# Optimization experiments

Measured on AMD Instinct MI355X. Metric: run time of the kernel, lower is better.

Reference implementation:

```python
import jax, jax.numpy as jnp
import numpy as np

EPS = 1e-12  # F.normalize default eps


def setup_inputs() -> dict:
    key = jax.random.key(0)
    k1, k2 = jax.random.split(key)
    E, N, B, T, Fdim, K = 2, 512, 64, 12, 2, 64
    supports = jax.random.uniform(k1, (E, N, N), dtype=jnp.float32)
    inputs = jax.random.normal(k2, (B, T, N, Fdim), dtype=jnp.float32)
    bias = jnp.ones((E, K), dtype=jnp.float32)  # init.ones_
    # torch.svd at __init__: A = u @ diag(s) @ v^T, truncated to node_dim
    u_np, s_np, vh_np = np.linalg.svd(np.asarray(supports), full_matrices=False)
    u = jnp.asarray(u_np[..., :K])                      # [E, N, K]
    s = jnp.asarray(s_np[..., :K])                      # [E, K]
    v = jnp.asarray(np.swapaxes(vh_np, -1, -2)[..., :K])  # [E, N, K]
    return {"supports": supports, "u": u, "s": s, "v": v, "bias": bias, "inputs": inputs}


def _pairwise_dist(x):
    # x: [B, N, T] L2-normalized rows; returns [B, N, N] Euclidean distances
    sq = jnp.sum(x * x, axis=-1)                      # [B, N]
    inner = jnp.einsum('bnt,bmt->bnm', x, x)          # [B, N, N]
    d2 = jnp.maximum(sq[:, :, None] + sq[:, None, :] - 2.0 * inner, 0.0)
    # safe sqrt (zero on the diagonal, matching torch.cdist)
    pos = d2 > 0
    return jnp.where(pos, jnp.sqrt(jnp.where(pos, d2, 1.0)), 0.0)


def reference(supports, u, s, v, bias, inputs):
    # SAdaptor: low-rank SVD reconstruction with softplus-scaled singular values
    s_scaled = s * jax.nn.softplus(bias)              # [E, K]
    adaptive = jnp.einsum('enk,ek,emk->enm', u, s_scaled, v)  # [E, N, N]
    sup = supports + adaptive                         # [E, N, N]

    # TAdaptor: exp(-cdist) of L2-normalized node histories (dropout: eval mode)
    x = jnp.transpose(inputs[..., 0], (0, 2, 1))      # [B, N, T]
    nrm = jnp.sqrt(jnp.sum(x * x, axis=-1, keepdims=True))
    nodes = x / jnp.maximum(nrm, EPS)                 # F.normalize(p=2)
    dynamic = jnp.exp(-_pairwise_dist(nodes))         # [B, N, N]

    out = sup[:, None, :, :] * (dynamic[None] + 1.0)  # [E, B, N, N]
    out = jax.nn.relu(out)
    # F.normalize(p=1, dim=-1); out >= 0 so |out| == out
    return out / jnp.maximum(jnp.sum(out, axis=-1, keepdims=True), EPS)
```

## Files before the change

kernel.cpp:

```cpp
#include <hip/hip_runtime.h>

#define E 2
#define N 512
#define B 64
#define T 12
#define K 64
#define NB 4

template<int CTRL, int RM>
__device__ __forceinline__ float dpp_add(float x) {
    int y = __builtin_amdgcn_update_dpp(0, __float_as_int(x), CTRL, RM, 0xf, true);
    return x + __int_as_float(y);
}
__device__ __forceinline__ float wave_sum64(float x) {
    x = dpp_add<0x111, 0xf>(x);
    x = dpp_add<0x112, 0xf>(x);
    x = dpp_add<0x114, 0xf>(x);
    x = dpp_add<0x118, 0xf>(x);
    x = dpp_add<0x142, 0xa>(x);
    x = dpp_add<0x143, 0xc>(x);
    return __int_as_float(__builtin_amdgcn_readlane(__float_as_int(x), 63));
}

__global__ __launch_bounds__(512)
void k_prep(const float* __restrict__ supports, const float* __restrict__ uu,
            const float* __restrict__ ss, const float* __restrict__ vv,
            const float* __restrict__ bias, const float* __restrict__ inp,
            float* __restrict__ sup, float* __restrict__ nodes) {
    const int blk = blockIdx.x;
    const int tid = threadIdx.x;
    if (blk < 2 * (N / NB)) {
        const int e = blk >> 7;
        const int n0 = (blk & 127) * NB;
        __shared__ float uls[NB][K];
        if (tid < NB * K) {
            const int j = tid >> 6, k = tid & 63;
            float bb = bias[e * K + k];
            float sp_ = (bb > 0.f) ? (bb + log1pf(expf(-bb))) : log1pf(expf(bb));
            uls[j][k] = uu[(size_t)(e * N + n0 + j) * K + k] * ss[e * K + k] * sp_;
        }
        __syncthreads();
        const int m = tid;
        const float4* vp = reinterpret_cast<const float4*>(vv + (size_t)(e * N + m) * K);
        float accs[NB] = {0.f, 0.f, 0.f, 0.f};
#pragma unroll
        for (int i = 0; i < 16; ++i) {
            float4 q = vp[i];
#pragma unroll
            for (int j = 0; j < NB; ++j) {
                const float* w = &uls[j][i * 4];
                accs[j] += w[0] * q.x + w[1] * q.y + w[2] * q.z + w[3] * q.w;
            }
        }
#pragma unroll
        for (int j = 0; j < NB; ++j) {
            const size_t o = (size_t)(e * N + n0 + j) * N + m;
            sup[o] = accs[j] + supports[o];
        }
    } else {
        const int idx = (blk - 2 * (N / NB)) * 512 + tid;
        const int b = idx >> 9, n = idx & (N - 1);
        float x[T];
        float sq = 0.f;
#pragma unroll
        for (int t = 0; t < T; ++t) {
            float xv = inp[((size_t)(b * T + t) * N + n) * 2];
            x[t] = xv;
            sq += xv * xv;
        }
        float inv = 1.f / fmaxf(sqrtf(sq), 1e-12f);
#pragma unroll
        for (int t = 0; t < T; ++t) nodes[(size_t)idx * T + t] = x[t] * inv;
    }
}

__global__ __launch_bounds__(512)
void k_main(const float* __restrict__ sup, const float* __restrict__ nodes,
            float* __restrict__ out) {
    const int bi = blockIdx.x;
    const int b = bi >> 7;
    const int n0 = (bi & 127) * NB;
    const int m = threadIdx.x;
    const int wave = m >> 6, lane = m & 63;

    __shared__ float red[8 * 8];
    __shared__ float invs[8];

    const float4* np4 = reinterpret_cast<const float4*>(nodes + (size_t)(b * N + m) * T);
    float4 q0 = np4[0], q1 = np4[1], q2 = np4[2];
    float r[T] = {q0.x, q0.y, q0.z, q0.w, q1.x, q1.y, q1.z, q1.w, q2.x, q2.y, q2.z, q2.w};

    const float* __restrict__ anc = nodes + (size_t)(b * N + n0) * T;

    float sp[NB][2];
#pragma unroll
    for (int j = 0; j < NB; ++j) {
        sp[j][0] = sup[(size_t)(n0 + j) * N + m];
        sp[j][1] = sup[(size_t)(N + n0 + j) * N + m];
    }

    float v[NB][2];
#pragma unroll
    for (int j = 0; j < NB; ++j) {
        float d2 = 0.f;
#pragma unroll
        for (int t = 0; t < T; ++t) {
            float d = r[t] - anc[j * T + t];
            d2 += d * d;
        }
        float dist = (d2 > 0.f) ? sqrtf(d2) : 0.f;
        float f = __expf(-dist) + 1.f;
        v[j][0] = fmaxf(sp[j][0] * f, 0.f);
        v[j][1] = fmaxf(sp[j][1] * f, 0.f);
    }

#pragma unroll
    for (int j = 0; j < NB; ++j) {
#pragma unroll
        for (int e = 0; e < 2; ++e) {
            float tot = wave_sum64(v[j][e]);
            if (lane == 0) red[wave * 8 + j * 2 + e] = tot;
        }
    }
    __syncthreads();
    if (wave == 0) {
        float t = red[lane];
        t += __shfl_xor(t, 8);
        t += __shfl_xor(t, 16);
        t += __shfl_xor(t, 32);
        if (lane < 8) invs[lane] = 1.f / fmaxf(t, 1e-12f);
    }
    __syncthreads();

#pragma unroll
    for (int j = 0; j < NB; ++j) {
#pragma unroll
        for (int e = 0; e < 2; ++e) {
            out[((size_t)(e * B + b) * N + n0 + j) * N + m] = v[j][e] * invs[j * 2 + e];
        }
    }
}

extern "C" void kernel_launch(void* const* d_in, const int* in_sizes, int n_in,
                              void* d_out, int out_size, void* d_ws, size_t ws_size,
                              hipStream_t stream) {
    const float* supports = (const float*)d_in[0];
    const float* uu       = (const float*)d_in[1];
    const float* ss       = (const float*)d_in[2];
    const float* vv       = (const float*)d_in[3];
    const float* bias     = (const float*)d_in[4];
    const float* inp      = (const float*)d_in[5];
    float* out = (float*)d_out;

    float* sup   = (float*)d_ws;
    float* nodes = sup + (size_t)E * N * N;

    k_prep<<<2 * (N / NB) + (B * N) / 512, 512, 0, stream>>>(
        supports, uu, ss, vv, bias, inp, sup, nodes);
    k_main<<<B * (N / NB), 512, 0, stream>>>(sup, nodes, out);
}
```

Before: 170.0 us.

## Remap k_main threads to one row per 128-thread group with float4 columns

Each 128-thread group now owns one anchor row and each thread handles four consecutive columns. Loads and stores become float4, the per-row reduction shrinks to two wave sums plus a single shared-memory step, and one of the two block barriers is removed. The cost is that every thread loads 48 node floats, so the redundant loads rise, and register pressure goes up.

```diff
diff --git a/kernel.cpp b/kernel.cpp
--- a/kernel.cpp
+++ b/kernel.cpp
@@ -80,65 +80,59 @@
     const int bi = blockIdx.x;
     const int b = bi >> 7;
     const int n0 = (bi & 127) * NB;
-    const int m = threadIdx.x;
-    const int wave = m >> 6, lane = m & 63;
+    const int t = threadIdx.x;
+    const int g = __builtin_amdgcn_readfirstlane(t >> 7);
+    const int m0 = (t & 127) * 4;
+    const int wave = t >> 6, lane = t & 63;
 
-    __shared__ float red[8 * 8];
-    __shared__ float invs[8];
+    __shared__ float red[8][2];
 
-    const float4* np4 = reinterpret_cast<const float4*>(nodes + (size_t)(b * N + m) * T);
-    float4 q0 = np4[0], q1 = np4[1], q2 = np4[2];
-    float r[T] = {q0.x, q0.y, q0.z, q0.w, q1.x, q1.y, q1.z, q1.w, q2.x, q2.y, q2.z, q2.w};
+    const float* __restrict__ anc = nodes + ((size_t)(b * N) + n0 + g) * T;
+    float a[T];
+#pragma unroll
+    for (int i = 0; i < T; ++i) a[i] = anc[i];
 
-    const float* __restrict__ anc = nodes + (size_t)(b * N + n0) * T;
+    const float4* np4 = reinterpret_cast<const float4*>(nodes + ((size_t)(b * N) + m0) * T);
+    float4 nr[12];
+#pragma unroll
+    for (int i = 0; i < 12; ++i) nr[i] = np4[i];
+    const float* x = reinterpret_cast<const float*>(nr);
 
-    float sp[NB][2];
+    float4 s0 = *reinterpret_cast<const float4*>(sup + (size_t)(n0 + g) * N + m0);
+    float4 s1 = *reinterpret_cast<const float4*>(sup + (size_t)N * N + (size_t)(n0 + g) * N + m0);
+    const float* sp0 = reinterpret_cast<const float*>(&s0);
+    const float* sp1 = reinterpret_cast<const float*>(&s1);
+
+    float v0[4], v1[4];
+    float ls0 = 0.f, ls1 = 0.f;
 #pragma unroll
-    for (int j = 0; j < NB; ++j) {
-        sp[j][0] = sup[(size_t)(n0 + j) * N + m];
-        sp[j][1] = sup[(size_t)(N + n0 + j) * N + m];
-    }
-
-    float v[NB][2];
-#pragma unroll
-    for (int j = 0; j < NB; ++j) {
+    for (int k = 0; k < 4; ++k) {
         float d2 = 0.f;
 #pragma unroll
-        for (int t = 0; t < T; ++t) {
-            float d = r[t] - anc[j * T + t];
+        for (int i = 0; i < T; ++i) {
+            float d = x[k * T + i] - a[i];
             d2 += d * d;
         }
         float dist = (d2 > 0.f) ? sqrtf(d2) : 0.f;
         float f = __expf(-dist) + 1.f;
-        v[j][0] = fmaxf(sp[j][0] * f, 0.f);
-        v[j][1] = fmaxf(sp[j][1] * f, 0.f);
+        v0[k] = fmaxf(sp0[k] * f, 0.f);
+        v1[k] = fmaxf(sp1[k] * f, 0.f);
+        ls0 += v0[k];
+        ls1 += v1[k];
     }
 
-#pragma unroll
-    for (int j = 0; j < NB; ++j) {
-#pragma unroll
-        for (int e = 0; e < 2; ++e) {
-            float tot = wave_sum64(v[j][e]);
-            if (lane == 0) red[wave * 8 + j * 2 + e] = tot;
-        }
-    }
-    __syncthreads();
-    if (wave == 0) {
-        float t = red[lane];
-        t += __shfl_xor(t, 8);
-        t += __shfl_xor(t, 16);
-        t += __shfl_xor(t, 32);
-        if (lane < 8) invs[lane] = 1.f / fmaxf(t, 1e-12f);
-    }
+    float w0 = wave_sum64(ls0);
+    float w1 = wave_sum64(ls1);
+    if (lane == 0) { red[wave][0] = w0; red[wave][1] = w1; }
     __syncthreads();
 
-#pragma unroll
-    for (int j = 0; j < NB; ++j) {
-#pragma unroll
-        for (int e = 0; e < 2; ++e) {
-            out[((size_t)(e * B + b) * N + n0 + j) * N + m] = v[j][e] * invs[j * 2 + e];
-        }
-    }
+    float inv0 = 1.f / fmaxf(red[2 * g][0] + red[2 * g + 1][0], 1e-12f);
+    float inv1 = 1.f / fmaxf(red[2 * g][1] + red[2 * g + 1][1], 1e-12f);
+
+    float4 o0 = make_float4(v0[0] * inv0, v0[1] * inv0, v0[2] * inv0, v0[3] * inv0);
+    float4 o1 = make_float4(v1[0] * inv1, v1[1] * inv1, v1[2] * inv1, v1[3] * inv1);
+    *reinterpret_cast<float4*>(out + ((size_t)(0 * B + b) * N + n0 + g) * N + m0) = o0;
+    *reinterpret_cast<float4*>(out + ((size_t)(1 * B + b) * N + n0 + g) * N + m0) = o1;
 }
 
 extern "C" void kernel_launch(void* const* d_in, const int* in_sizes, int n_in,
```

New measurement: 190.0 us. 1.12x slower.
